# Kernel optimization log

Measured on AMD Instinct MI355X. Metric: run time of the kernel, lower is better.

## Reference

```python
import jax, jax.numpy as jnp
import numpy as np

SMALL = -1000.0

def _crf_loss(pred, transitions, tags, seq_len):
    B, T, L = pred.shape
    START, STOP = L - 2, L - 1
    # pred[:, :, -2] = pred[:, :, -1] = small
    pred = pred.at[:, :, START].set(SMALL).at[:, :, STOP].set(SMALL)
    # start / end padding states
    start_state = jnp.full((B, 1, L), SMALL, pred.dtype).at[:, :, START].set(0.0)
    end_state = jnp.zeros((B, 1, L), pred.dtype)
    padded = jnp.concatenate([start_state, pred, end_state], axis=1)  # [B, T+2, L]
    b_idx = jnp.arange(B)
    padded = padded.at[b_idx, seq_len + 1, :].set(SMALL)
    padded = padded.at[b_idx, seq_len + 1, STOP].set(0.0)
    padded_t = jnp.transpose(padded, (1, 0, 2))  # [T+2, B, L]

    def step(prev, emit):
        # prev: [B, L] (from-label), emit: [B, L] (to-label)
        new = jax.nn.logsumexp(prev[:, :, None] + transitions[None, :, :] + emit[:, None, :], axis=1)
        return new, new

    _, alphas = jax.lax.scan(step, padded_t[0], padded_t[1:])  # [T+1, B, L]
    gathered = alphas[seq_len, b_idx, :]  # [B, L] (alphas at position seq_len)
    pred_paths_scores = jnp.sum(jax.nn.logsumexp(gathered, axis=1))

    # real path emission score
    pos = jnp.arange(T)
    mask = (pos[None, :] < seq_len[:, None]).astype(pred.dtype)  # [B, T]
    emit_score = jnp.take_along_axis(pred, tags[:, :, None], axis=2)[:, :, 0]  # [B, T]
    real_path_score = jnp.sum(emit_score * mask)

    # real path transition score
    start_tag = jnp.full((B, 1), START, tags.dtype)
    end_tag = jnp.zeros((B, 1), tags.dtype)
    padded_tags = jnp.concatenate([start_tag, tags, end_tag], axis=1)  # [B, T+2]
    padded_tags = padded_tags.at[b_idx, seq_len + 1].set(STOP)
    trans_score = transitions[padded_tags[:, :-1], padded_tags[:, 1:]]  # [B, T+1]
    tpos = jnp.arange(T + 1)
    tmask = (tpos[None, :] < (seq_len + 1)[:, None]).astype(pred.dtype)
    real_path_score = real_path_score + jnp.sum(trans_score * tmask)

    return pred_paths_scores - real_path_score


def setup_inputs() -> dict:
    key = jax.random.key(0)
    k1, k2, k3, k4 = jax.random.split(key, 4)
    B, T, L = 128, 1024, 128
    pred = jax.random.normal(k1, (B, T, L), dtype=jnp.float32)
    transitions = jax.random.normal(k2, (L, L), dtype=jnp.float32) * 0.1
    tags = jax.random.randint(k3, (B, T), 0, L - 2)  # real labels only, [0, L-3]
    seq_len = jax.random.randint(k4, (B,), 1, T + 1)
    return {"pred": pred, "transitions": transitions, "tags": tags, "seq_len": seq_len}


def reference(pred, transitions, tags, seq_len):
    return _crf_loss(pred, transitions, tags, seq_len)
```

## Files before the change

kernel.cpp:

```cpp
#include <hip/hip_runtime.h>

constexpr int L      = 128;
constexpr int TDIM   = 1024;
constexpr int NBATCH = 128;
constexpr int START  = L - 2;
constexpr int STOP   = L - 1;
constexpr int BSUB   = 16;
constexpr int NBLK   = NBATCH / BSUB;

typedef short bf16x8 __attribute__((ext_vector_type(8)));
typedef float f32x4  __attribute__((ext_vector_type(4)));
typedef int   i32x4  __attribute__((ext_vector_type(4)));

union B4 { i32x4 i; bf16x8 v; };

__device__ __forceinline__ short f2bf(float f) {
    unsigned x = __float_as_uint(f);
    return (short)((x + 0x7fffu + ((x >> 16) & 1u)) >> 16);
}
__device__ __forceinline__ unsigned pkbf(float lo, float hi) {
    unsigned r;
    asm("v_cvt_pk_bf16_f32 %0, %1, %2" : "=v"(r) : "v"(lo), "v"(hi));
    return r;
}

__global__ __launch_bounds__(256)
void crf_pexp(const float* __restrict__ pred, const int* __restrict__ seq_len,
              unsigned short* __restrict__ pexp)
{
    int gid  = blockIdx.x * 256 + threadIdx.x;
    int lane = gid & 63;
    int c    = (gid >> 6) & 3;
    int row  = (gid >> 8) & 1023;
    int blk  = gid >> 18;
    int l15 = lane & 15, l4 = lane >> 4;
    int b = blk * 16 + l15;
    bool live = row < seq_len[b];

    const float* src = pred + ((size_t)b * TDIM + row) * L + 32 * c + 4 * l4;
    f32x4 v0 = *(const f32x4*)(src);
    f32x4 v1 = *(const f32x4*)(src + 16);

    float e0[4], e1[4];
#pragma unroll
    for (int r = 0; r < 4; ++r) {
        int s0 = 32 * c + 4 * l4 + r;
        int s1 = s0 + 16;
        e0[r] = (live && s0 < 126) ? __expf(v0[r]) : 0.0f;
        e1[r] = (live && s1 < 126) ? __expf(v1[r]) : 0.0f;
    }
    i32x4 out;
    out[0] = (int)pkbf(e0[0], e0[1]);
    out[1] = (int)pkbf(e0[2], e0[3]);
    out[2] = (int)pkbf(e1[0], e1[1]);
    out[3] = (int)pkbf(e1[2], e1[3]);
    *(i32x4*)((char*)pexp + (size_t)gid * 16) = out;
}

struct PB { i32x4 c[4]; };
struct PF { f32x4 q[8]; };

#define STAGE(TA, TB, ACCIN, PBUF, CHK, SCL)                                 \
  {                                                                          \
    unsigned wa0 = (unsigned)PBUF.c[(TA) >> 1][((TA) & 1) * 2 + 0];          \
    unsigned wa1 = (unsigned)PBUF.c[(TA) >> 1][((TA) & 1) * 2 + 1];          \
    unsigned wb0 = (unsigned)PBUF.c[(TB) >> 1][((TB) & 1) * 2 + 0];          \
    unsigned wb1 = (unsigned)PBUF.c[(TB) >> 1][((TB) & 1) * 2 + 1];          \
    float ua0 = ACCIN[TA][0] * __uint_as_float(wa0 << 16);                   \
    float ua1 = ACCIN[TA][1] * __uint_as_float(wa0 & 0xffff0000u);           \
    float ua2 = ACCIN[TA][2] * __uint_as_float(wa1 << 16);                   \
    float ua3 = ACCIN[TA][3] * __uint_as_float(wa1 & 0xffff0000u);           \
    float ub0 = ACCIN[TB][0] * __uint_as_float(wb0 << 16);                   \
    float ub1 = ACCIN[TB][1] * __uint_as_float(wb0 & 0xffff0000u);           \
    float ub2 = ACCIN[TB][2] * __uint_as_float(wb1 << 16);                   \
    float ub3 = ACCIN[TB][3] * __uint_as_float(wb1 & 0xffff0000u);           \
    if ((SCL) && applyScale) {                                               \
      ua0 *= 0x1p-64f; ua1 *= 0x1p-64f; ua2 *= 0x1p-64f; ua3 *= 0x1p-64f;    \
      ub0 *= 0x1p-64f; ub1 *= 0x1p-64f; ub2 *= 0x1p-64f; ub3 *= 0x1p-64f;    \
    }                                                                        \
    if (CHK) {                                                               \
      mloc = fmaxf(mloc, fmaxf(fmaxf(fmaxf(ua0, ua1), fmaxf(ua2, ua3)),      \
                               fmaxf(fmaxf(ub0, ub1), fmaxf(ub2, ub3))));    \
    }                                                                        \
    B[TA].i[0] = (int)pkbf(ua0, ua1);                                        \
    B[TA].i[1] = (int)pkbf(ua2, ua3);                                        \
    B[TA].i[2] = (int)pkbf(ub0, ub1);                                        \
    B[TA].i[3] = (int)pkbf(ub2, ub3);                                        \
    __builtin_amdgcn_sched_group_barrier(0x002, 20, 0);                      \
  }

#define GROUP(ACCO, KT, SEED)                                                \
  {                                                                          \
    ACCO[0] = __builtin_amdgcn_mfma_f32_16x16x32_bf16(A[0][KT], B[KT].v, (SEED) ? Z4 : ACCO[0], 0, 0, 0); \
    ACCO[4] = __builtin_amdgcn_mfma_f32_16x16x32_bf16(A[4][KT], B[KT].v, (SEED) ? Z4 : ACCO[4], 0, 0, 0); \
    ACCO[1] = __builtin_amdgcn_mfma_f32_16x16x32_bf16(A[1][KT], B[KT].v, (SEED) ? Z4 : ACCO[1], 0, 0, 0); \
    ACCO[5] = __builtin_amdgcn_mfma_f32_16x16x32_bf16(A[5][KT], B[KT].v, (SEED) ? Z4 : ACCO[5], 0, 0, 0); \
    ACCO[2] = __builtin_amdgcn_mfma_f32_16x16x32_bf16(A[2][KT], B[KT].v, (SEED) ? Z4 : ACCO[2], 0, 0, 0); \
    ACCO[6] = __builtin_amdgcn_mfma_f32_16x16x32_bf16(A[6][KT], B[KT].v, (SEED) ? Z4 : ACCO[6], 0, 0, 0); \
    ACCO[3] = __builtin_amdgcn_mfma_f32_16x16x32_bf16(A[3][KT], B[KT].v, (SEED) ? Z4 : ACCO[3], 0, 0, 0); \
    ACCO[7] = __builtin_amdgcn_mfma_f32_16x16x32_bf16(A[7][KT], B[KT].v, (SEED) ? Z4 : ACCO[7], 0, 0, 0); \
    __builtin_amdgcn_sched_group_barrier(0x008, 8, 0);                       \
  }

#define ITER(T_, ACCIN, ACCOUT, PBUF, CHK, SCL)                              \
  {                                                                          \
    const int tS = (T_);                                                     \
    float mloc = 0.0f; (void)mloc;                                           \
    STAGE(0, 4, ACCIN, PBUF, CHK, SCL)                                       \
    STAGE(1, 5, ACCIN, PBUF, CHK, SCL)                                       \
    GROUP(ACCOUT, 0, true)                                                   \
    STAGE(2, 6, ACCIN, PBUF, CHK, SCL)                                       \
    GROUP(ACCOUT, 1, false)                                                  \
    STAGE(3, 7, ACCIN, PBUF, CHK, SCL)                                       \
    { bool hit = (tS == srow1);                                              \
      res  = hit ? ACCIN[7][3] : res;                                        \
      resC = hit ? C : resC; }                                               \
    if ((SCL) && applyScale) { C += 44.3614195558365f; applyScale = false; } \
    GROUP(ACCOUT, 2, false)                                                  \
    GROUP(ACCOUT, 3, false)                                                  \
    if (CHK) applyScale = (__ballot(mloc > 0x1p80f) != 0ull);                \
    loadPB(PBUF, min(tS + 1, TDIM - 1));                                     \
  }

template<bool PEXP>
__global__ __launch_bounds__(64, 1)
void crf_chain(const float* __restrict__ pred,
               const float* __restrict__ trans,
               const int* __restrict__ seq_len,
               const unsigned short* __restrict__ pexp,
               float* __restrict__ fwd_out)
{
    const int lane = threadIdx.x;
    const int l15 = lane & 15, l4 = lane >> 4;
    const int blk = blockIdx.x;
    const int b   = blk * BSUB + l15;

    bf16x8 A[8][4];
#pragma unroll
    for (int T = 0; T < 8; ++T)
#pragma unroll
        for (int kt = 0; kt < 4; ++kt) {
            bf16x8 v;
#pragma unroll
            for (int e = 0; e < 8; ++e) {
                int s = 16 * kt + 64 * (e >> 2) + 4 * l4 + (e & 3);
                v[e] = f2bf(__expf(trans[s * L + 16 * T + l15]));
            }
            A[T][kt] = v;
        }

    const int srow1 = seq_len[b] + 1;

    int mx = srow1;
#pragma unroll
    for (int d = 1; d < 16; d <<= 1) mx = max(mx, __shfl_xor(mx, d));
    const int tmaxR = __builtin_amdgcn_readfirstlane((mx + 1) & ~1);

    B4 B[4];
#pragma unroll
    for (int kt = 0; kt < 4; ++kt) B[kt].i = (i32x4){0, 0, 0, 0};
    if (l4 == 3) B[3].i[3] = 0x3F80;

    const f32x4 Z4 = {0.f, 0.f, 0.f, 0.f};

    float C = 0.0f;
    bool  applyScale = false;
    float res = 1.0f, resC = 0.0f;

    const char*  pxb = (const char*)pexp + (size_t)blk * 1024 * 4096;
    const float* pfb = pred + (size_t)b * TDIM * L + 4 * l4;

    auto loadPB = [&](PB& p, int row) {
        const i32x4* s = (const i32x4*)(pxb + (size_t)row * 4096) + lane;
        p.c[0] = s[0]; p.c[1] = s[64]; p.c[2] = s[128]; p.c[3] = s[192];
    };
    auto loadPF = [&](PF& p, int row) {
        const f32x4* s = (const f32x4*)(pfb + (size_t)row * L);
#pragma unroll
        for (int T = 0; T < 8; ++T) p.q[T] = s[T * 4];
    };

    if constexpr (PEXP) {
        PB pa, pb_;
        loadPB(pa, 0); loadPB(pb_, 1);

        f32x4 accX[8], accY[8];
        GROUP(accX, 0, true)
        GROUP(accX, 1, false)
        GROUP(accX, 2, false)
        GROUP(accX, 3, false)

        for (int t0 = 1; t0 < tmaxR; t0 += 2) {
            ITER(t0,     accX, accY, pa,  true,  false)
            ITER(t0 + 1, accY, accX, pb_, false, true)
        }
    } else {
        PF fa, fb;
        loadPF(fa, 0); loadPF(fb, 1);
        f32x4 acc[8];
        auto stepF = [&](int t, PF& pf, bool chk) {
#pragma unroll
            for (int T = 0; T < 8; ++T)
                acc[T] = __builtin_amdgcn_mfma_f32_16x16x32_bf16(A[T][0], B[0].v, Z4, 0, 0, 0);
#pragma unroll
            for (int kt = 1; kt < 4; ++kt)
#pragma unroll
                for (int T = 0; T < 8; ++T)
                    acc[T] = __builtin_amdgcn_mfma_f32_16x16x32_bf16(A[T][kt], B[kt].v, acc[T], 0, 0, 0);

            bool hit = (t == srow1);
            res  = hit ? acc[7][3] : res;
            resC = hit ? C : resC;

            const bool live = (t < srow1);
            float u[8][4];
#pragma unroll
            for (int T = 0; T < 8; ++T)
#pragma unroll
                for (int r = 0; r < 4; ++r) {
                    bool dead = !live || (T == 7 && l4 == 3 && r >= 2);
                    u[T][r] = dead ? 0.0f : acc[T][r] * __expf(pf.q[T][r]);
                }
            if (applyScale) {
#pragma unroll
                for (int T = 0; T < 8; ++T)
#pragma unroll
                    for (int r = 0; r < 4; ++r) u[T][r] *= 0x1p-64f;
                C += 44.3614195558365f;
            }
            applyScale = false;
            if (chk) {
                float m[8];
#pragma unroll
                for (int T = 0; T < 8; ++T)
                    m[T] = fmaxf(fmaxf(u[T][0], u[T][1]), fmaxf(u[T][2], u[T][3]));
                float mx4 = fmaxf(fmaxf(fmaxf(m[0], m[1]), fmaxf(m[2], m[3])),
                                  fmaxf(fmaxf(m[4], m[5]), fmaxf(m[6], m[7])));
                applyScale = (__ballot(mx4 > 0x1p80f) != 0ull);
            }
#pragma unroll
            for (int kt = 0; kt < 4; ++kt) {
                B[kt].i[0] = (int)pkbf(u[kt][0], u[kt][1]);
                B[kt].i[1] = (int)pkbf(u[kt][2], u[kt][3]);
                B[kt].i[2] = (int)pkbf(u[kt + 4][0], u[kt + 4][1]);
                B[kt].i[3] = (int)pkbf(u[kt + 4][2], u[kt + 4][3]);
            }
            loadPF(pf, min(t + 1, TDIM - 1));
        };
        for (int t0 = 0; t0 < tmaxR; t0 += 2) {
            stepF(t0 + 1, fa, true);
            stepF(t0 + 2, fb, false);
        }
    }

    if (l4 == 3)
        fwd_out[b] = __logf(res) + resC;
}

__global__ __launch_bounds__(256)
void crf_score(const float* __restrict__ pred,
               const float* __restrict__ trans,
               const int* __restrict__ tags,
               const int* __restrict__ seq_len,
               float* __restrict__ score_out)
{
    const int b = blockIdx.x;
    const int tid = threadIdx.x;
    const int sl = seq_len[b];
    const int* tg = tags + b * TDIM;

    float s = 0.0f;
    for (int t = tid; t < sl; t += 256) {
        int tag = tg[t];
        s += pred[((long)b * TDIM + t) * L + tag];
        int prev = (t == 0) ? START : tg[t - 1];
        s += trans[prev * L + tag];
    }
    if (tid == 0) s += trans[tg[sl - 1] * L + STOP];

    __shared__ float red[4];
#pragma unroll
    for (int d = 1; d < 64; d <<= 1) s += __shfl_xor(s, d);
    if ((tid & 63) == 0) red[tid >> 6] = s;
    __syncthreads();
    if (tid == 0) score_out[b] = (red[0] + red[1]) + (red[2] + red[3]);
}

__global__ __launch_bounds__(128)
void crf_combine(const float* __restrict__ fwd,
                 const float* __restrict__ real,
                 float* __restrict__ out)
{
    const int tid = threadIdx.x;
    float s = fwd[tid] - real[tid];
#pragma unroll
    for (int d = 1; d < 64; d <<= 1) s += __shfl_xor(s, d);
    __shared__ float red[2];
    if ((tid & 63) == 0) red[tid >> 6] = s;
    __syncthreads();
    if (tid == 0) out[0] = red[0] + red[1];
}

extern "C" void kernel_launch(void* const* d_in, const int* in_sizes, int n_in,
                              void* d_out, int out_size, void* d_ws, size_t ws_size,
                              hipStream_t stream)
{
    const float* pred    = (const float*)d_in[0];
    const float* trans   = (const float*)d_in[1];
    const int*   tags    = (const int*)d_in[2];
    const int*   seq_len = (const int*)d_in[3];

    float* ws   = (float*)d_ws;
    float* fwd  = ws;
    float* real = ws + 128;

    const size_t pexp_bytes = (size_t)NBLK * 1024 * 4096;
    if (ws_size >= 1024 + pexp_bytes) {
        unsigned short* pexp = (unsigned short*)((char*)d_ws + 1024);
        crf_pexp<<<8192, 256, 0, stream>>>(pred, seq_len, pexp);
        crf_chain<true><<<NBLK, 64, 0, stream>>>(pred, trans, seq_len, pexp, fwd);
    } else {
        crf_chain<false><<<NBLK, 64, 0, stream>>>(pred, trans, seq_len, nullptr, fwd);
    }
    crf_score  <<<NBATCH, 256, 0, stream>>>(pred, trans, tags, seq_len, real);
    crf_combine<<<1, 128, 0, stream>>>(fwd, real, (float*)d_out);
}
```

Before: 480.5 us.

## Split MFMA accumulation into two independent K-half chains and check overflow every step

Each step's MFMA accumulation is split into two independent accumulator sets covering even and odd K halves, summed at the start of the next stage. This roughly halves the dependent MFMA chain length on the serial recurrence critical path. The overflow rescale check now runs every step through precomputed scale-factor and offset registers instead of alternating check and apply steps. In exchange it costs extra accumulator registers and vector adds, plus a ballot on every step.

New measurement: 674.0 us. +40.3%, slower.

```diff
diff --git a/kernel.cpp b/kernel.cpp
--- a/kernel.cpp
+++ b/kernel.cpp
@@ -60,65 +60,81 @@
 struct PB { i32x4 c[4]; };
 struct PF { f32x4 q[8]; };
 
-#define STAGE(TA, TB, ACCIN, PBUF, CHK, SCL)                                 \
+#define STAGE2(KT, INE, INO, PBUF)                                           \
   {                                                                          \
-    unsigned wa0 = (unsigned)PBUF.c[(TA) >> 1][((TA) & 1) * 2 + 0];          \
-    unsigned wa1 = (unsigned)PBUF.c[(TA) >> 1][((TA) & 1) * 2 + 1];          \
-    unsigned wb0 = (unsigned)PBUF.c[(TB) >> 1][((TB) & 1) * 2 + 0];          \
-    unsigned wb1 = (unsigned)PBUF.c[(TB) >> 1][((TB) & 1) * 2 + 1];          \
-    float ua0 = ACCIN[TA][0] * __uint_as_float(wa0 << 16);                   \
-    float ua1 = ACCIN[TA][1] * __uint_as_float(wa0 & 0xffff0000u);           \
-    float ua2 = ACCIN[TA][2] * __uint_as_float(wa1 << 16);                   \
-    float ua3 = ACCIN[TA][3] * __uint_as_float(wa1 & 0xffff0000u);           \
-    float ub0 = ACCIN[TB][0] * __uint_as_float(wb0 << 16);                   \
-    float ub1 = ACCIN[TB][1] * __uint_as_float(wb0 & 0xffff0000u);           \
-    float ub2 = ACCIN[TB][2] * __uint_as_float(wb1 << 16);                   \
-    float ub3 = ACCIN[TB][3] * __uint_as_float(wb1 & 0xffff0000u);           \
-    if ((SCL) && applyScale) {                                               \
-      ua0 *= 0x1p-64f; ua1 *= 0x1p-64f; ua2 *= 0x1p-64f; ua3 *= 0x1p-64f;    \
-      ub0 *= 0x1p-64f; ub1 *= 0x1p-64f; ub2 *= 0x1p-64f; ub3 *= 0x1p-64f;    \
+    f32x4 sA = INE[KT] + INO[KT];                                            \
+    f32x4 sB = INE[(KT) + 4] + INO[(KT) + 4];                                \
+    if ((KT) == 3) {                                                         \
+      bool hit = (tS == srow1);                                              \
+      res  = hit ? sB[3] : res;                                              \
+      resC = hit ? C : resC;                                                 \
     }                                                                        \
-    if (CHK) {                                                               \
-      mloc = fmaxf(mloc, fmaxf(fmaxf(fmaxf(ua0, ua1), fmaxf(ua2, ua3)),      \
-                               fmaxf(fmaxf(ub0, ub1), fmaxf(ub2, ub3))));    \
-    }                                                                        \
-    B[TA].i[0] = (int)pkbf(ua0, ua1);                                        \
-    B[TA].i[1] = (int)pkbf(ua2, ua3);                                        \
-    B[TA].i[2] = (int)pkbf(ub0, ub1);                                        \
-    B[TA].i[3] = (int)pkbf(ub2, ub3);                                        \
-    __builtin_amdgcn_sched_group_barrier(0x002, 20, 0);                      \
+    unsigned wa0 = (unsigned)PBUF.c[(KT) >> 1][((KT) & 1) * 2 + 0];          \
+    unsigned wa1 = (unsigned)PBUF.c[(KT) >> 1][((KT) & 1) * 2 + 1];          \
+    unsigned wb0 = (unsigned)PBUF.c[((KT) + 4) >> 1][(((KT) + 4) & 1) * 2 + 0]; \
+    unsigned wb1 = (unsigned)PBUF.c[((KT) + 4) >> 1][(((KT) + 4) & 1) * 2 + 1]; \
+    float p0 = __uint_as_float(wa0 << 16) * sfac;                            \
+    float p1 = __uint_as_float(wa0 & 0xffff0000u) * sfac;                    \
+    float p2 = __uint_as_float(wa1 << 16) * sfac;                            \
+    float p3 = __uint_as_float(wa1 & 0xffff0000u) * sfac;                    \
+    float q0 = __uint_as_float(wb0 << 16) * sfac;                            \
+    float q1 = __uint_as_float(wb0 & 0xffff0000u) * sfac;                    \
+    float q2 = __uint_as_float(wb1 << 16) * sfac;                            \
+    float q3 = __uint_as_float(wb1 & 0xffff0000u) * sfac;                    \
+    float ua0 = sA[0] * p0, ua1 = sA[1] * p1;                                \
+    float ua2 = sA[2] * p2, ua3 = sA[3] * p3;                                \
+    float ub0 = sB[0] * q0, ub1 = sB[1] * q1;                                \
+    float ub2 = sB[2] * q2, ub3 = sB[3] * q3;                                \
+    mloc = fmaxf(mloc, fmaxf(fmaxf(fmaxf(ua0, ua1), fmaxf(ua2, ua3)),        \
+                             fmaxf(fmaxf(ub0, ub1), fmaxf(ub2, ub3))));      \
+    B[KT].i[0] = (int)pkbf(ua0, ua1);                                        \
+    B[KT].i[1] = (int)pkbf(ua2, ua3);                                        \
+    B[KT].i[2] = (int)pkbf(ub0, ub1);                                        \
+    B[KT].i[3] = (int)pkbf(ub2, ub3);                                        \
+    __builtin_amdgcn_sched_group_barrier(0x002, 24, 0);                      \
   }
 
-#define GROUP(ACCO, KT, SEED)                                                \
+#define GRP_SEED(OUT, KT)                                                    \
   {                                                                          \
-    ACCO[0] = __builtin_amdgcn_mfma_f32_16x16x32_bf16(A[0][KT], B[KT].v, (SEED) ? Z4 : ACCO[0], 0, 0, 0); \
-    ACCO[4] = __builtin_amdgcn_mfma_f32_16x16x32_bf16(A[4][KT], B[KT].v, (SEED) ? Z4 : ACCO[4], 0, 0, 0); \
-    ACCO[1] = __builtin_amdgcn_mfma_f32_16x16x32_bf16(A[1][KT], B[KT].v, (SEED) ? Z4 : ACCO[1], 0, 0, 0); \
-    ACCO[5] = __builtin_amdgcn_mfma_f32_16x16x32_bf16(A[5][KT], B[KT].v, (SEED) ? Z4 : ACCO[5], 0, 0, 0); \
-    ACCO[2] = __builtin_amdgcn_mfma_f32_16x16x32_bf16(A[2][KT], B[KT].v, (SEED) ? Z4 : ACCO[2], 0, 0, 0); \
-    ACCO[6] = __builtin_amdgcn_mfma_f32_16x16x32_bf16(A[6][KT], B[KT].v, (SEED) ? Z4 : ACCO[6], 0, 0, 0); \
-    ACCO[3] = __builtin_amdgcn_mfma_f32_16x16x32_bf16(A[3][KT], B[KT].v, (SEED) ? Z4 : ACCO[3], 0, 0, 0); \
-    ACCO[7] = __builtin_amdgcn_mfma_f32_16x16x32_bf16(A[7][KT], B[KT].v, (SEED) ? Z4 : ACCO[7], 0, 0, 0); \
+    OUT[0] = __builtin_amdgcn_mfma_f32_16x16x32_bf16(A[0][KT], B[KT].v, Z4, 0, 0, 0); \
+    OUT[4] = __builtin_amdgcn_mfma_f32_16x16x32_bf16(A[4][KT], B[KT].v, Z4, 0, 0, 0); \
+    OUT[1] = __builtin_amdgcn_mfma_f32_16x16x32_bf16(A[1][KT], B[KT].v, Z4, 0, 0, 0); \
+    OUT[5] = __builtin_amdgcn_mfma_f32_16x16x32_bf16(A[5][KT], B[KT].v, Z4, 0, 0, 0); \
+    OUT[2] = __builtin_amdgcn_mfma_f32_16x16x32_bf16(A[2][KT], B[KT].v, Z4, 0, 0, 0); \
+    OUT[6] = __builtin_amdgcn_mfma_f32_16x16x32_bf16(A[6][KT], B[KT].v, Z4, 0, 0, 0); \
+    OUT[3] = __builtin_amdgcn_mfma_f32_16x16x32_bf16(A[3][KT], B[KT].v, Z4, 0, 0, 0); \
+    OUT[7] = __builtin_amdgcn_mfma_f32_16x16x32_bf16(A[7][KT], B[KT].v, Z4, 0, 0, 0); \
     __builtin_amdgcn_sched_group_barrier(0x008, 8, 0);                       \
   }
-
-#define ITER(T_, ACCIN, ACCOUT, PBUF, CHK, SCL)                              \
+#define GRP_ACC(OUT, KT)                                                     \
+  {                                                                          \
+    OUT[0] = __builtin_amdgcn_mfma_f32_16x16x32_bf16(A[0][KT], B[KT].v, OUT[0], 0, 0, 0); \
+    OUT[4] = __builtin_amdgcn_mfma_f32_16x16x32_bf16(A[4][KT], B[KT].v, OUT[4], 0, 0, 0); \
+    OUT[1] = __builtin_amdgcn_mfma_f32_16x16x32_bf16(A[1][KT], B[KT].v, OUT[1], 0, 0, 0); \
+    OUT[5] = __builtin_amdgcn_mfma_f32_16x16x32_bf16(A[5][KT], B[KT].v, OUT[5], 0, 0, 0); \
+    OUT[2] = __builtin_amdgcn_mfma_f32_16x16x32_bf16(A[2][KT], B[KT].v, OUT[2], 0, 0, 0); \
+    OUT[6] = __builtin_amdgcn_mfma_f32_16x16x32_bf16(A[6][KT], B[KT].v, OUT[6], 0, 0, 0); \
+    OUT[3] = __builtin_amdgcn_mfma_f32_16x16x32_bf16(A[3][KT], B[KT].v, OUT[3], 0, 0, 0); \
+    OUT[7] = __builtin_amdgcn_mfma_f32_16x16x32_bf16(A[7][KT], B[KT].v, OUT[7], 0, 0, 0); \
+    __builtin_amdgcn_sched_group_barrier(0x008, 8, 0);                       \
+  }
+
+#define ITER(T_, INE, INO, OE, OO, PBUF)                                     \
   {                                                                          \
     const int tS = (T_);                                                     \
-    float mloc = 0.0f; (void)mloc;                                           \
-    STAGE(0, 4, ACCIN, PBUF, CHK, SCL)                                       \
-    STAGE(1, 5, ACCIN, PBUF, CHK, SCL)                                       \
-    GROUP(ACCOUT, 0, true)                                                   \
-    STAGE(2, 6, ACCIN, PBUF, CHK, SCL)                                       \
-    GROUP(ACCOUT, 1, false)                                                  \
-    STAGE(3, 7, ACCIN, PBUF, CHK, SCL)                                       \
-    { bool hit = (tS == srow1);                                              \
-      res  = hit ? ACCIN[7][3] : res;                                        \
-      resC = hit ? C : resC; }                                               \
-    if ((SCL) && applyScale) { C += 44.3614195558365f; applyScale = false; } \
-    GROUP(ACCOUT, 2, false)                                                  \
-    GROUP(ACCOUT, 3, false)                                                  \
-    if (CHK) applyScale = (__ballot(mloc > 0x1p80f) != 0ull);                \
+    float mloc = 0.0f;                                                       \
+    STAGE2(0, INE, INO, PBUF)                                                \
+    STAGE2(1, INE, INO, PBUF)                                                \
+    GRP_SEED(OE, 0)                                                          \
+    STAGE2(2, INE, INO, PBUF)                                                \
+    GRP_SEED(OO, 2)                                                          \
+    STAGE2(3, INE, INO, PBUF)                                                \
+    C += cadd;                                                               \
+    GRP_ACC(OE, 1)                                                           \
+    GRP_ACC(OO, 3)                                                           \
+    bool tr = (__ballot(mloc > 0x1p80f) != 0ull);                            \
+    sfac = tr ? 0x1p-64f : 1.0f;                                             \
+    cadd = tr ? 44.3614195558365f : 0.0f;                                    \
     loadPB(PBUF, min(tS + 1, TDIM - 1));                                     \
   }
 
@@ -164,7 +180,7 @@
     const f32x4 Z4 = {0.f, 0.f, 0.f, 0.f};
 
     float C = 0.0f;
-    bool  applyScale = false;
+    float sfac = 1.0f, cadd = 0.0f;
     float res = 1.0f, resC = 0.0f;
 
     const char*  pxb = (const char*)pexp + (size_t)blk * 1024 * 4096;
@@ -184,20 +200,21 @@
         PB pa, pb_;
         loadPB(pa, 0); loadPB(pb_, 1);
 
-        f32x4 accX[8], accY[8];
-        GROUP(accX, 0, true)
-        GROUP(accX, 1, false)
-        GROUP(accX, 2, false)
-        GROUP(accX, 3, false)
+        f32x4 XE[8], XO[8], YE[8], YO[8];
+        GRP_SEED(XE, 0)
+        GRP_ACC (XE, 1)
+        GRP_SEED(XO, 2)
+        GRP_ACC (XO, 3)
 
         for (int t0 = 1; t0 < tmaxR; t0 += 2) {
-            ITER(t0,     accX, accY, pa,  true,  false)
-            ITER(t0 + 1, accY, accX, pb_, false, true)
+            ITER(t0,     XE, XO, YE, YO, pa )
+            ITER(t0 + 1, YE, YO, XE, XO, pb_)
         }
     } else {
         PF fa, fb;
         loadPF(fa, 0); loadPF(fb, 1);
         f32x4 acc[8];
+        bool applyScale = false;
         auto stepF = [&](int t, PF& pf, bool chk) {
 #pragma unroll
             for (int T = 0; T < 8; ++T)
```

## Interleave two independent batch chains per wave in the forward recurrence

Applied to the files above, without the earlier changes.

The forward-scan kernel now handles two 16-batch sub-blocks per wavefront, alternating phases between chain A and chain B. Each chain's elementwise stage then overlaps with the other chain's MFMA group, hiding the serial dependency latency of a single chain. The launch grid drops from 8 blocks to 4, so fewer CUs are busy, and register pressure roughly doubles for accumulators and B operands. The scan length for both chains is now set by the longer of the two sub-blocks.

Measured after the change: 957.3 us. 1.99x slower.

```diff
diff --git a/kernel.cpp b/kernel.cpp
--- a/kernel.cpp
+++ b/kernel.cpp
@@ -60,80 +60,79 @@
 struct PB { i32x4 c[4]; };
 struct PF { f32x4 q[8]; };
 
-#define STAGE(TA, TB, ACCIN, PBUF, CHK, SCL)                                 \
+#define GRP(ACCO, KT, BS, SEED)                                              \
+  {                                                                          \
+    ACCO[0] = __builtin_amdgcn_mfma_f32_16x16x32_bf16(A[0][KT], BS[KT].v, (SEED) ? Z4 : ACCO[0], 0, 0, 0); \
+    ACCO[4] = __builtin_amdgcn_mfma_f32_16x16x32_bf16(A[4][KT], BS[KT].v, (SEED) ? Z4 : ACCO[4], 0, 0, 0); \
+    ACCO[1] = __builtin_amdgcn_mfma_f32_16x16x32_bf16(A[1][KT], BS[KT].v, (SEED) ? Z4 : ACCO[1], 0, 0, 0); \
+    ACCO[5] = __builtin_amdgcn_mfma_f32_16x16x32_bf16(A[5][KT], BS[KT].v, (SEED) ? Z4 : ACCO[5], 0, 0, 0); \
+    ACCO[2] = __builtin_amdgcn_mfma_f32_16x16x32_bf16(A[2][KT], BS[KT].v, (SEED) ? Z4 : ACCO[2], 0, 0, 0); \
+    ACCO[6] = __builtin_amdgcn_mfma_f32_16x16x32_bf16(A[6][KT], BS[KT].v, (SEED) ? Z4 : ACCO[6], 0, 0, 0); \
+    ACCO[3] = __builtin_amdgcn_mfma_f32_16x16x32_bf16(A[3][KT], BS[KT].v, (SEED) ? Z4 : ACCO[3], 0, 0, 0); \
+    ACCO[7] = __builtin_amdgcn_mfma_f32_16x16x32_bf16(A[7][KT], BS[KT].v, (SEED) ? Z4 : ACCO[7], 0, 0, 0); \
+    __builtin_amdgcn_sched_group_barrier(0x008, 8, 0);                       \
+  }
+
+#define STG(TA, TB, AIN, PBUF, BT, CHK, SCL, APS, MLOC)                      \
   {                                                                          \
     unsigned wa0 = (unsigned)PBUF.c[(TA) >> 1][((TA) & 1) * 2 + 0];          \
     unsigned wa1 = (unsigned)PBUF.c[(TA) >> 1][((TA) & 1) * 2 + 1];          \
     unsigned wb0 = (unsigned)PBUF.c[(TB) >> 1][((TB) & 1) * 2 + 0];          \
     unsigned wb1 = (unsigned)PBUF.c[(TB) >> 1][((TB) & 1) * 2 + 1];          \
-    float ua0 = ACCIN[TA][0] * __uint_as_float(wa0 << 16);                   \
-    float ua1 = ACCIN[TA][1] * __uint_as_float(wa0 & 0xffff0000u);           \
-    float ua2 = ACCIN[TA][2] * __uint_as_float(wa1 << 16);                   \
-    float ua3 = ACCIN[TA][3] * __uint_as_float(wa1 & 0xffff0000u);           \
-    float ub0 = ACCIN[TB][0] * __uint_as_float(wb0 << 16);                   \
-    float ub1 = ACCIN[TB][1] * __uint_as_float(wb0 & 0xffff0000u);           \
-    float ub2 = ACCIN[TB][2] * __uint_as_float(wb1 << 16);                   \
-    float ub3 = ACCIN[TB][3] * __uint_as_float(wb1 & 0xffff0000u);           \
-    if ((SCL) && applyScale) {                                               \
+    float ua0 = AIN[TA][0] * __uint_as_float(wa0 << 16);                     \
+    float ua1 = AIN[TA][1] * __uint_as_float(wa0 & 0xffff0000u);             \
+    float ua2 = AIN[TA][2] * __uint_as_float(wa1 << 16);                     \
+    float ua3 = AIN[TA][3] * __uint_as_float(wa1 & 0xffff0000u);             \
+    float ub0 = AIN[TB][0] * __uint_as_float(wb0 << 16);                     \
+    float ub1 = AIN[TB][1] * __uint_as_float(wb0 & 0xffff0000u);             \
+    float ub2 = AIN[TB][2] * __uint_as_float(wb1 << 16);                     \
+    float ub3 = AIN[TB][3] * __uint_as_float(wb1 & 0xffff0000u);             \
+    if ((SCL) && APS) {                                                      \
       ua0 *= 0x1p-64f; ua1 *= 0x1p-64f; ua2 *= 0x1p-64f; ua3 *= 0x1p-64f;    \
       ub0 *= 0x1p-64f; ub1 *= 0x1p-64f; ub2 *= 0x1p-64f; ub3 *= 0x1p-64f;    \
     }                                                                        \
     if (CHK) {                                                               \
-      mloc = fmaxf(mloc, fmaxf(fmaxf(fmaxf(ua0, ua1), fmaxf(ua2, ua3)),      \
+      MLOC = fmaxf(MLOC, fmaxf(fmaxf(fmaxf(ua0, ua1), fmaxf(ua2, ua3)),      \
                                fmaxf(fmaxf(ub0, ub1), fmaxf(ub2, ub3))));    \
     }                                                                        \
-    B[TA].i[0] = (int)pkbf(ua0, ua1);                                        \
-    B[TA].i[1] = (int)pkbf(ua2, ua3);                                        \
-    B[TA].i[2] = (int)pkbf(ub0, ub1);                                        \
-    B[TA].i[3] = (int)pkbf(ub2, ub3);                                        \
+    BT[TA].i[0] = (int)pkbf(ua0, ua1);                                       \
+    BT[TA].i[1] = (int)pkbf(ua2, ua3);                                       \
+    BT[TA].i[2] = (int)pkbf(ub0, ub1);                                       \
+    BT[TA].i[3] = (int)pkbf(ub2, ub3);                                       \
     __builtin_amdgcn_sched_group_barrier(0x002, 20, 0);                      \
   }
 
-#define GROUP(ACCO, KT, SEED)                                                \
-  {                                                                          \
-    ACCO[0] = __builtin_amdgcn_mfma_f32_16x16x32_bf16(A[0][KT], B[KT].v, (SEED) ? Z4 : ACCO[0], 0, 0, 0); \
-    ACCO[4] = __builtin_amdgcn_mfma_f32_16x16x32_bf16(A[4][KT], B[KT].v, (SEED) ? Z4 : ACCO[4], 0, 0, 0); \
-    ACCO[1] = __builtin_amdgcn_mfma_f32_16x16x32_bf16(A[1][KT], B[KT].v, (SEED) ? Z4 : ACCO[1], 0, 0, 0); \
-    ACCO[5] = __builtin_amdgcn_mfma_f32_16x16x32_bf16(A[5][KT], B[KT].v, (SEED) ? Z4 : ACCO[5], 0, 0, 0); \
-    ACCO[2] = __builtin_amdgcn_mfma_f32_16x16x32_bf16(A[2][KT], B[KT].v, (SEED) ? Z4 : ACCO[2], 0, 0, 0); \
-    ACCO[6] = __builtin_amdgcn_mfma_f32_16x16x32_bf16(A[6][KT], B[KT].v, (SEED) ? Z4 : ACCO[6], 0, 0, 0); \
-    ACCO[3] = __builtin_amdgcn_mfma_f32_16x16x32_bf16(A[3][KT], B[KT].v, (SEED) ? Z4 : ACCO[3], 0, 0, 0); \
-    ACCO[7] = __builtin_amdgcn_mfma_f32_16x16x32_bf16(A[7][KT], B[KT].v, (SEED) ? Z4 : ACCO[7], 0, 0, 0); \
-    __builtin_amdgcn_sched_group_barrier(0x008, 8, 0);                       \
-  }
-
-#define ITER(T_, ACCIN, ACCOUT, PBUF, CHK, SCL)                              \
+#define PHASE(T_, AIN, AOUT, PBUF, BT, BS, CHK, SCL, APS, CV, RES, RESC, SROW, PXB) \
   {                                                                          \
     const int tS = (T_);                                                     \
     float mloc = 0.0f; (void)mloc;                                           \
-    STAGE(0, 4, ACCIN, PBUF, CHK, SCL)                                       \
-    STAGE(1, 5, ACCIN, PBUF, CHK, SCL)                                       \
-    GROUP(ACCOUT, 0, true)                                                   \
-    STAGE(2, 6, ACCIN, PBUF, CHK, SCL)                                       \
-    GROUP(ACCOUT, 1, false)                                                  \
-    STAGE(3, 7, ACCIN, PBUF, CHK, SCL)                                       \
-    { bool hit = (tS == srow1);                                              \
-      res  = hit ? ACCIN[7][3] : res;                                        \
-      resC = hit ? C : resC; }                                               \
-    if ((SCL) && applyScale) { C += 44.3614195558365f; applyScale = false; } \
-    GROUP(ACCOUT, 2, false)                                                  \
-    GROUP(ACCOUT, 3, false)                                                  \
-    if (CHK) applyScale = (__ballot(mloc > 0x1p80f) != 0ull);                \
-    loadPB(PBUF, min(tS + 1, TDIM - 1));                                     \
+    STG(0, 4, AIN, PBUF, BT, CHK, SCL, APS, mloc)                            \
+    GRP(AOUT, 0, BS, true)                                                   \
+    STG(1, 5, AIN, PBUF, BT, CHK, SCL, APS, mloc)                            \
+    GRP(AOUT, 1, BS, false)                                                  \
+    STG(2, 6, AIN, PBUF, BT, CHK, SCL, APS, mloc)                            \
+    GRP(AOUT, 2, BS, false)                                                  \
+    STG(3, 7, AIN, PBUF, BT, CHK, SCL, APS, mloc)                            \
+    { bool hit = (tS == (SROW));                                             \
+      RES  = hit ? AIN[7][3] : RES;                                          \
+      RESC = hit ? CV : RESC; }                                              \
+    if ((SCL) && APS) { CV += 44.3614195558365f; APS = false; }              \
+    GRP(AOUT, 3, BS, false)                                                  \
+    if (CHK) APS = (__ballot(mloc > 0x1p80f) != 0ull);                       \
+    loadPB(PBUF, min(tS, TDIM - 1), PXB);                                    \
   }
 
-template<bool PEXP>
+template<int MODE>
 __global__ __launch_bounds__(64, 1)
 void crf_chain(const float* __restrict__ pred,
                const float* __restrict__ trans,
                const int* __restrict__ seq_len,
-               const unsigned short* __restrict__ pexp,
+               const void* __restrict__ px,
                float* __restrict__ fwd_out)
 {
     const int lane = threadIdx.x;
     const int l15 = lane & 15, l4 = lane >> 4;
     const int blk = blockIdx.x;
-    const int b   = blk * BSUB + l15;
 
     bf16x8 A[8][4];
 #pragma unroll
@@ -149,53 +148,85 @@
             A[T][kt] = v;
         }
 
-    const int srow1 = seq_len[b] + 1;
-
-    int mx = srow1;
-#pragma unroll
-    for (int d = 1; d < 16; d <<= 1) mx = max(mx, __shfl_xor(mx, d));
-    const int tmaxR = __builtin_amdgcn_readfirstlane((mx + 1) & ~1);
-
-    B4 B[4];
-#pragma unroll
-    for (int kt = 0; kt < 4; ++kt) B[kt].i = (i32x4){0, 0, 0, 0};
-    if (l4 == 3) B[3].i[3] = 0x3F80;
-
     const f32x4 Z4 = {0.f, 0.f, 0.f, 0.f};
 
-    float C = 0.0f;
-    bool  applyScale = false;
-    float res = 1.0f, resC = 0.0f;
-
-    const char*  pxb = (const char*)pexp + (size_t)blk * 1024 * 4096;
-    const float* pfb = pred + (size_t)b * TDIM * L + 4 * l4;
-
-    auto loadPB = [&](PB& p, int row) {
+    auto loadPB = [&](PB& p, int row, const char* pxb) {
         const i32x4* s = (const i32x4*)(pxb + (size_t)row * 4096) + lane;
         p.c[0] = s[0]; p.c[1] = s[64]; p.c[2] = s[128]; p.c[3] = s[192];
     };
-    auto loadPF = [&](PF& p, int row) {
-        const f32x4* s = (const f32x4*)(pfb + (size_t)row * L);
-#pragma unroll
-        for (int T = 0; T < 8; ++T) p.q[T] = s[T * 4];
-    };
-
-    if constexpr (PEXP) {
-        PB pa, pb_;
-        loadPB(pa, 0); loadPB(pb_, 1);
-
-        f32x4 accX[8], accY[8];
-        GROUP(accX, 0, true)
-        GROUP(accX, 1, false)
-        GROUP(accX, 2, false)
-        GROUP(accX, 3, false)
+
+    if constexpr (MODE == 1) {
+        const int bA = blk * 32 + l15;
+        const int bB = blk * 32 + 16 + l15;
+        const char* pxbA = (const char*)px + ((size_t)(2 * blk) << 22);
+        const char* pxbB = (const char*)px + ((size_t)(2 * blk + 1) << 22);
+
+        const int srow1A = seq_len[bA] + 1;
+        const int srow1B = seq_len[bB] + 1;
+
+        int mx = max(srow1A, srow1B);
+#pragma unroll
+        for (int d = 1; d < 16; d <<= 1) mx = max(mx, __shfl_xor(mx, d));
+        const int tmaxR = __builtin_amdgcn_readfirstlane((mx + 1) & ~1);
+
+        B4 B_A[4], B_B[4];
+#pragma unroll
+        for (int kt = 0; kt < 4; ++kt) {
+            B_A[kt].i = (i32x4){0, 0, 0, 0};
+            B_B[kt].i = (i32x4){0, 0, 0, 0};
+        }
+        if (l4 == 3) { B_A[3].i[3] = 0x3F80; B_B[3].i[3] = 0x3F80; }
+
+        float CA = 0.0f, CB = 0.0f;
+        bool  apsA = false, apsB = false;
+        float resA = 1.0f, resCA = 0.0f, resB = 1.0f, resCB = 0.0f;
+
+        PB pA, pB;
+        loadPB(pA, 0, pxbA);
+        loadPB(pB, 0, pxbB);
+
+        f32x4 accA[8], accB[8];
+        GRP(accA, 0, B_A, true)
+        GRP(accA, 1, B_A, false)
+        GRP(accA, 2, B_A, false)
+        GRP(accA, 3, B_A, false)
 
         for (int t0 = 1; t0 < tmaxR; t0 += 2) {
-            ITER(t0,     accX, accY, pa,  true,  false)
-            ITER(t0 + 1, accY, accX, pb_, false, true)
+            PHASE(t0, accA, accB, pA, B_A, B_B, true, false, apsA, CA, resA, resCA, srow1A, pxbA)
+            PHASE(t0, accB, accA, pB, B_B, B_A, true, false, apsB, CB, resB, resCB, srow1B, pxbB)
+            PHASE(t0 + 1, accA, accB, pA, B_A, B_B, false, true, apsA, CA, resA, resCA, srow1A, pxbA)
+            PHASE(t0 + 1, accB, accA, pB, B_B, B_A, false, true, apsB, CB, resB, resCB, srow1B, pxbB)
+        }
+
+        if (l4 == 3) {
+            fwd_out[bA] = __logf(resA) + resCA;
+            fwd_out[bB] = __logf(resB) + resCB;
         }
     } else {
+        const int b = blk * BSUB + l15;
+        const int srow1 = seq_len[b] + 1;
+
+        int mx = srow1;
+#pragma unroll
+        for (int d = 1; d < 16; d <<= 1) mx = max(mx, __shfl_xor(mx, d));
+        const int tmaxR = __builtin_amdgcn_readfirstlane((mx + 1) & ~1);
+
+        B4 B[4];
+#pragma unroll
+        for (int kt = 0; kt < 4; ++kt) B[kt].i = (i32x4){0, 0, 0, 0};
+        if (l4 == 3) B[3].i[3] = 0x3F80;
+
+        float C = 0.0f;
+        bool  applyScale = false;
+        float res = 1.0f, resC = 0.0f;
+
+        const float* pfb = pred + (size_t)b * TDIM * L + 4 * l4;
         PF fa, fb;
+        auto loadPF = [&](PF& p, int row) {
+            const f32x4* s = (const f32x4*)(pfb + (size_t)row * L);
+#pragma unroll
+            for (int T = 0; T < 8; ++T) p.q[T] = s[T * 4];
+        };
         loadPF(fa, 0); loadPF(fb, 1);
         f32x4 acc[8];
         auto stepF = [&](int t, PF& pf, bool chk) {
@@ -251,10 +282,9 @@
             stepF(t0 + 1, fa, true);
             stepF(t0 + 2, fb, false);
         }
+        if (l4 == 3)
+            fwd_out[b] = __logf(res) + resC;
     }
-
-    if (l4 == 3)
-        fwd_out[b] = __logf(res) + resC;
 }
 
 __global__ __launch_bounds__(256)
@@ -314,13 +344,14 @@
     float* fwd  = ws;
     float* real = ws + 128;
 
-    const size_t pexp_bytes = (size_t)NBLK * 1024 * 4096;
-    if (ws_size >= 1024 + pexp_bytes) {
-        unsigned short* pexp = (unsigned short*)((char*)d_ws + 1024);
-        crf_pexp<<<8192, 256, 0, stream>>>(pred, seq_len, pexp);
-        crf_chain<true><<<NBLK, 64, 0, stream>>>(pred, trans, seq_len, pexp, fwd);
+    const size_t bf16_bytes = (size_t)NBLK * 1024 * 4096;
+    void* pxbuf = (char*)d_ws + 1024;
+
+    if (ws_size >= 1024 + bf16_bytes) {
+        crf_pexp<<<8192, 256, 0, stream>>>(pred, seq_len, (unsigned short*)pxbuf);
+        crf_chain<1><<<4, 64, 0, stream>>>(pred, trans, seq_len, pxbuf, fwd);
     } else {
-        crf_chain<false><<<NBLK, 64, 0, stream>>>(pred, trans, seq_len, nullptr, fwd);
+        crf_chain<0><<<NBLK, 64, 0, stream>>>(pred, trans, seq_len, nullptr, fwd);
     }
     crf_score  <<<NBATCH, 256, 0, stream>>>(pred, trans, tags, seq_len, real);
     crf_combine<<<1, 128, 0, stream>>>(fwd, real, (float*)d_out);
```
